# Optimization experiments

Measured on AMD Instinct MI355X. Metric: run time of the kernel, lower is better.

The kernel has to match this reference:

```python
import jax, jax.numpy as jnp
import numpy as np

N_NODES = 20000
N_EDGES = 320000
HID = 128          # hidden_dim
IN_DIM = 192       # edge_rep feature dim
NODE_IN = 64       # node_feature dim


def _w(key, shape, fan_in):
    return jax.random.normal(key, shape, dtype=jnp.float32) * (1.0 / np.sqrt(fan_in))


def setup_inputs() -> dict:
    key = jax.random.key(0)
    ks = jax.random.split(key, 16)
    edge_index = jax.random.randint(ks[0], (2, N_EDGES), 0, N_NODES)
    edge_rep = jax.random.normal(ks[1], (N_EDGES, IN_DIM), dtype=jnp.float32)
    x = jax.random.normal(ks[2], (N_NODES, HID), dtype=jnp.float32)
    prototype = jax.random.normal(ks[3], (N_NODES, HID), dtype=jnp.float32)
    node_feature = jax.random.normal(ks[4], (N_NODES, NODE_IN), dtype=jnp.float32)
    # incidence: each graph edge belongs to the hyperedges of its two endpoint nodes
    inc_edge = jnp.concatenate([jnp.arange(N_EDGES), jnp.arange(N_EDGES)])      # indexes graph edges (conv 'nodes')
    inc_hyper = jnp.concatenate([edge_index[0], edge_index[1]])                 # indexes nodes (hyperedges)
    hyper_edge = jnp.stack([inc_edge, inc_hyper])                               # [2, 2E]
    return {
        "edge_index": edge_index,
        "edge_rep": edge_rep,
        "x": x,
        "hyper_edge": hyper_edge,
        "prototype": prototype,
        "node_feature": node_feature,
        "lin1_W": _w(ks[5], (2 * HID, HID), 2 * HID),
        "lin1_b": jnp.zeros((HID,), jnp.float32),
        "lin2_W": _w(ks[6], (HID, 1), HID),
        "lin2_b": jnp.zeros((1,), jnp.float32),
        "hc1_W": _w(ks[7], (2 * HID, 2 * HID), 2 * HID),
        "hc1_b": jnp.zeros((2 * HID,), jnp.float32),
        "hc2_W": _w(ks[8], (2 * HID, HID), 2 * HID),
        "hc2_b": jnp.zeros((HID,), jnp.float32),
    }


def hyperconv(xh, inc_n, inc_e, w, W, b, n_nodes, n_hyper):
    # X' = D^{-1} H B H^T (X W) + b, with D_i = sum of incidence weights at node i,
    # B_e = 1/|e| (hyperedge degree normalization).
    xh = xh @ W                                                       # [n_nodes, out]
    D = jax.ops.segment_sum(w[:, 0], inc_n, num_segments=n_nodes)
    Dinv = jnp.where(D > 0, 1.0 / D, 0.0)
    B = jax.ops.segment_sum(jnp.ones_like(w[:, 0]), inc_e, num_segments=n_hyper)
    Binv = jnp.where(B > 0, 1.0 / B, 0.0)
    e = jax.ops.segment_sum(Binv[inc_e][:, None] * xh[inc_n], inc_e, num_segments=n_hyper)
    out = Dinv[:, None] * jax.ops.segment_sum(e[inc_n * 0 + inc_e] if False else e[inc_e], inc_n, num_segments=n_nodes)
    return out + b


def reference(edge_index, edge_rep, x, hyper_edge, prototype, node_feature,
              lin1_W, lin1_b, lin2_W, lin2_b, hc1_W, hc1_b, hc2_W, hc2_b):
    E = edge_rep.shape[0]
    N = x.shape[0]
    # gather-concat edge features
    f_u = node_feature[edge_index[0]]
    f_v = node_feature[edge_index[1]]
    er = jnp.concatenate([edge_rep, (f_u + f_v) * 0.5], axis=1)       # [E, 2*HID]
    # per-node scalar weight MLP (dropout = identity in eval mode)
    h = jax.nn.relu(jnp.concatenate([x, prototype], axis=-1) @ lin1_W + lin1_b)
    node_weight = jax.nn.sigmoid(h @ lin2_W + lin2_b)                 # [N, 1]
    hyper_w = node_weight[hyper_edge[1]]                              # [2E, 1] per-incidence weight
    inc_n, inc_e = hyper_edge[0], hyper_edge[1]
    er = jax.nn.sigmoid(hyperconv(er, inc_n, inc_e, hyper_w, hc1_W, hc1_b, E, N))
    er = jax.nn.sigmoid(hyperconv(er, inc_n, inc_e, hyper_w, hc2_W, hc2_b, E, N))
    return er
```

## Files before the change

### kernel.cpp

```cpp
#include <hip/hip_runtime.h>
#include <math.h>

#define NN 20000
#define NE 320000
#define HID 128
#define IN_DIM 192
#define NODE_IN 64

__device__ __forceinline__ float sigmoidf(float x) {
    return __builtin_amdgcn_rcpf(1.0f + __expf(-x));
}

template<bool CONCAT_A, bool RELU, bool BIAS>
__launch_bounds__(256)
__global__ void gemm_f32(const float* __restrict__ A0, const float* __restrict__ A1,
                         const float* __restrict__ B, const float* __restrict__ bias,
                         float* __restrict__ C, int M, int N, int K)
{
    __shared__ float As[16][68];
    __shared__ float Bs[16][68];
    const int tid = threadIdx.x;
    const int tx = tid & 15;
    const int ty = tid >> 4;
    const int m0 = blockIdx.x * 64;
    const int n0 = blockIdx.y * 64;
    float acc[4][4] = {};

    for (int k0 = 0; k0 < K; k0 += 16) {
        #pragma unroll
        for (int i = 0; i < 4; ++i) {
            int g = tid + i * 256;
            int r = g >> 4;
            int c = g & 15;
            int mr = m0 + r;
            int k  = k0 + c;
            float v = 0.f;
            if (mr < M) {
                if (CONCAT_A) v = (k < 128) ? A0[mr * 128 + k] : A1[mr * 128 + (k - 128)];
                else          v = A0[mr * K + k];
            }
            As[c][r] = v;
        }
        #pragma unroll
        for (int i = 0; i < 4; ++i) {
            int g = tid + i * 256;
            int kr = g >> 6;
            int c  = g & 63;
            Bs[kr][c] = B[(k0 + kr) * N + (n0 + c)];
        }
        __syncthreads();
        #pragma unroll
        for (int kk = 0; kk < 16; ++kk) {
            float4 a = *(const float4*)&As[kk][ty * 4];
            float4 b = *(const float4*)&Bs[kk][tx * 4];
            float av[4] = {a.x, a.y, a.z, a.w};
            float bv[4] = {b.x, b.y, b.z, b.w};
            #pragma unroll
            for (int i = 0; i < 4; ++i)
                #pragma unroll
                for (int j = 0; j < 4; ++j)
                    acc[i][j] = fmaf(av[i], bv[j], acc[i][j]);
        }
        __syncthreads();
    }
    #pragma unroll
    for (int i = 0; i < 4; ++i) {
        int row = m0 + ty * 4 + i;
        if (row < M) {
            #pragma unroll
            for (int j = 0; j < 4; ++j) {
                int col = n0 + tx * 4 + j;
                float v = acc[i][j];
                if (BIAS) v += bias[col];
                if (RELU) v = fmaxf(v, 0.f);
                C[row * N + col] = v;
            }
        }
    }
}

__global__ void nw_kernel(const float* __restrict__ h, const float* __restrict__ W2,
                          const float* __restrict__ b2, float* __restrict__ nw)
{
    int n = blockIdx.x * 4 + (threadIdx.x >> 6);
    int l = threadIdx.x & 63;
    if (n >= NN) return;
    float p = h[n * 128 + l] * W2[l] + h[n * 128 + 64 + l] * W2[64 + l];
    #pragma unroll
    for (int off = 32; off > 0; off >>= 1)
        p += __shfl_down(p, off, 64);
    if (l == 0) nw[n] = sigmoidf(p + b2[0]);
}

__global__ void deg_kernel(const int* __restrict__ ei, int* __restrict__ deg)
{
    int s = blockIdx.x * blockDim.x + threadIdx.x;
    if (s >= 2 * NE) return;
    atomicAdd(&deg[ei[s]], 1);
}

__global__ void dinv_kernel(const int* __restrict__ ei, const float* __restrict__ nw,
                            float* __restrict__ Dinv)
{
    int j = blockIdx.x * blockDim.x + threadIdx.x;
    if (j >= NE) return;
    float d = nw[ei[j]] + nw[ei[NE + j]];
    Dinv[j] = __builtin_amdgcn_rcpf(d);
}

__global__ void scan_kernel(const int* __restrict__ deg, int* __restrict__ off,
                            float* __restrict__ Binv)
{
    __shared__ int part[1024];
    int t = threadIdx.x;
    const int C = (NN + 1023) / 1024;
    int base = t * C;
    int s = 0;
    for (int i = 0; i < C; ++i) {
        int idx = base + i;
        if (idx < NN) s += deg[idx];
    }
    part[t] = s;
    __syncthreads();
    for (int o = 1; o < 1024; o <<= 1) {
        int v = (t >= o) ? part[t - o] : 0;
        __syncthreads();
        part[t] += v;
        __syncthreads();
    }
    int excl = (t == 0) ? 0 : part[t - 1];
    for (int i = 0; i < C; ++i) {
        int idx = base + i;
        if (idx < NN) {
            off[idx] = excl;
            int d = deg[idx];
            excl += d;
            Binv[idx] = (d > 0) ? 1.0f / (float)d : 0.0f;
        }
    }
    if (t == 0) off[NN] = part[1023];
}

__global__ void fill_kernel(const int* __restrict__ ei, const int* __restrict__ off,
                            int* __restrict__ cur, int* __restrict__ csr_j,
                            int* __restrict__ csr_o)
{
    int s = blockIdx.x * blockDim.x + threadIdx.x;
    if (s >= 2 * NE) return;
    int n = ei[s];
    int j = (s < NE) ? s : s - NE;
    int o = ei[(s < NE) ? s + NE : s - NE];
    int p = atomicAdd(&cur[n], 1);
    int w = off[n] + p;
    csr_j[w] = j;
    csr_o[w] = o;
}

__launch_bounds__(256)
__global__ void agg0_kernel(const int* __restrict__ csr_j, const int* __restrict__ csr_o,
                            const int* __restrict__ off, const float* __restrict__ Binv,
                            const float* __restrict__ er, const float* __restrict__ nf,
                            float* __restrict__ agg0)
{
    __shared__ int sh_j[256];
    __shared__ int sh_o[256];
    int n = blockIdx.x;
    int c = threadIdx.x;
    int s0 = off[n], s1 = off[n + 1];
    float a0 = 0.f, a1 = 0.f, a2 = 0.f, a3 = 0.f;
    for (int base = s0; base < s1; base += 256) {
        int cnt = min(256, s1 - base);
        if (c < cnt) {
            sh_j[c] = csr_j[base + c];
            sh_o[c] = csr_o[base + c];
        }
        __syncthreads();
        int t = 0;
        if (c < 192) {
            for (; t + 8 <= cnt; t += 8) {
                float v0 = er[sh_j[t + 0] * 192 + c];
                float v1 = er[sh_j[t + 1] * 192 + c];
                float v2 = er[sh_j[t + 2] * 192 + c];
                float v3 = er[sh_j[t + 3] * 192 + c];
                float v4 = er[sh_j[t + 4] * 192 + c];
                float v5 = er[sh_j[t + 5] * 192 + c];
                float v6 = er[sh_j[t + 6] * 192 + c];
                float v7 = er[sh_j[t + 7] * 192 + c];
                a0 += v0 + v4; a1 += v1 + v5; a2 += v2 + v6; a3 += v3 + v7;
            }
            for (; t < cnt; ++t) a0 += er[sh_j[t] * 192 + c];
        } else {
            int cc = c - 192;
            for (; t + 8 <= cnt; t += 8) {
                float v0 = nf[sh_o[t + 0] * 64 + cc];
                float v1 = nf[sh_o[t + 1] * 64 + cc];
                float v2 = nf[sh_o[t + 2] * 64 + cc];
                float v3 = nf[sh_o[t + 3] * 64 + cc];
                float v4 = nf[sh_o[t + 4] * 64 + cc];
                float v5 = nf[sh_o[t + 5] * 64 + cc];
                float v6 = nf[sh_o[t + 6] * 64 + cc];
                float v7 = nf[sh_o[t + 7] * 64 + cc];
                a0 += v0 + v4; a1 += v1 + v5; a2 += v2 + v6; a3 += v3 + v7;
            }
            for (; t < cnt; ++t) a0 += nf[sh_o[t] * 64 + cc];
        }
        __syncthreads();
    }
    float tot = (a0 + a1) + (a2 + a3);
    if (c >= 192) {
        float deg = (float)(s1 - s0);
        tot = 0.5f * (tot + deg * nf[n * 64 + (c - 192)]);
    }
    agg0[n * 256 + c] = tot * Binv[n];
}

__launch_bounds__(256)
__global__ void agg1_kernel(const int* __restrict__ csr_j, const int* __restrict__ csr_o,
                            const int* __restrict__ off, const float* __restrict__ Binv,
                            const float* __restrict__ Dinv, const float* __restrict__ e1,
                            const float* __restrict__ b1, float* __restrict__ agg1)
{
    __shared__ int sh_o[256];
    __shared__ float sh_d[256];
    int n = blockIdx.x;
    int c = threadIdx.x;
    int s0 = off[n], s1 = off[n + 1];
    float myv = e1[n * 256 + c];
    float bc = b1[c];
    float a0 = 0.f, a1 = 0.f, a2 = 0.f, a3 = 0.f;
    for (int base = s0; base < s1; base += 256) {
        int cnt = min(256, s1 - base);
        if (c < cnt) {
            int jj = csr_j[base + c];
            sh_o[c] = csr_o[base + c];
            sh_d[c] = Dinv[jj];
        }
        __syncthreads();
        int t = 0;
        for (; t + 8 <= cnt; t += 8) {
            float v0 = e1[sh_o[t + 0] * 256 + c];
            float v1 = e1[sh_o[t + 1] * 256 + c];
            float v2 = e1[sh_o[t + 2] * 256 + c];
            float v3 = e1[sh_o[t + 3] * 256 + c];
            float v4 = e1[sh_o[t + 4] * 256 + c];
            float v5 = e1[sh_o[t + 5] * 256 + c];
            float v6 = e1[sh_o[t + 6] * 256 + c];
            float v7 = e1[sh_o[t + 7] * 256 + c];
            a0 += sigmoidf(fmaf(sh_d[t + 0], myv + v0, bc));
            a1 += sigmoidf(fmaf(sh_d[t + 1], myv + v1, bc));
            a2 += sigmoidf(fmaf(sh_d[t + 2], myv + v2, bc));
            a3 += sigmoidf(fmaf(sh_d[t + 3], myv + v3, bc));
            a0 += sigmoidf(fmaf(sh_d[t + 4], myv + v4, bc));
            a1 += sigmoidf(fmaf(sh_d[t + 5], myv + v5, bc));
            a2 += sigmoidf(fmaf(sh_d[t + 6], myv + v6, bc));
            a3 += sigmoidf(fmaf(sh_d[t + 7], myv + v7, bc));
        }
        for (; t < cnt; ++t) {
            float v = e1[sh_o[t] * 256 + c];
            a0 += sigmoidf(fmaf(sh_d[t], myv + v, bc));
        }
        __syncthreads();
    }
    agg1[n * 256 + c] = ((a0 + a1) + (a2 + a3)) * Binv[n];
}

__global__ void out_kernel(const float* __restrict__ e2, const float* __restrict__ Dinv,
                           const int* __restrict__ ei, const float* __restrict__ b2,
                           float* __restrict__ out)
{
    int j = blockIdx.x * 2 + (threadIdx.x >> 7);
    int c = threadIdx.x & 127;
    int u = ei[j], v = ei[NE + j];
    float x = Dinv[j] * (e2[u * 128 + c] + e2[v * 128 + c]) + b2[c];
    out[j * 128 + c] = sigmoidf(x);
}

extern "C" void kernel_launch(void* const* d_in, const int* in_sizes, int n_in,
                              void* d_out, int out_size, void* d_ws, size_t ws_size,
                              hipStream_t stream)
{
    const int*   ei       = (const int*)  d_in[0];
    const float* edge_rep = (const float*)d_in[1];
    const float* x        = (const float*)d_in[2];
    const float* proto    = (const float*)d_in[4];
    const float* nf       = (const float*)d_in[5];
    const float* lin1_W   = (const float*)d_in[6];
    const float* lin1_b   = (const float*)d_in[7];
    const float* lin2_W   = (const float*)d_in[8];
    const float* lin2_b   = (const float*)d_in[9];
    const float* hc1_W    = (const float*)d_in[10];
    const float* hc1_b    = (const float*)d_in[11];
    const float* hc2_W    = (const float*)d_in[12];
    const float* hc2_b    = (const float*)d_in[13];
    float* out = (float*)d_out;

    const int S = 2 * NE;

    char* ws = (char*)d_ws;
    float* nw   = (float*)(ws);
    float* Dinv = (float*)(ws + 81920);
    int*   deg  = (int*)  (ws + 1363968);
    int*   off  = (int*)  (ws + 1445888);
    int*   cur  = (int*)  (ws + 1527808);
    float* Binv = (float*)(ws + 1609728);
    float* e2   = (float*)(ws + 1691648);

    char* ob = (char*)d_out;
    float* agg   = (float*)(ob);
    float* e1    = (float*)(ob + 20971520);
    float* h     = (float*)(ob + 41943040);
    int*   csr_j = (int*)  (ob + 52428800);
    int*   csr_o = (int*)  (ob + 54988800);

    hipMemsetAsync(deg, 0, NN * sizeof(int), stream);
    hipMemsetAsync(cur, 0, NN * sizeof(int), stream);

    gemm_f32<true, true, true><<<dim3(313, 2), 256, 0, stream>>>(
        x, proto, lin1_W, lin1_b, h, NN, 128, 256);

    nw_kernel<<<5000, 256, 0, stream>>>(h, lin2_W, lin2_b, nw);

    deg_kernel<<<(S + 255) / 256, 256, 0, stream>>>(ei, deg);

    dinv_kernel<<<(NE + 255) / 256, 256, 0, stream>>>(ei, nw, Dinv);

    scan_kernel<<<1, 1024, 0, stream>>>(deg, off, Binv);

    fill_kernel<<<(S + 255) / 256, 256, 0, stream>>>(ei, off, cur, csr_j, csr_o);

    agg0_kernel<<<NN, 256, 0, stream>>>(csr_j, csr_o, off, Binv, edge_rep, nf, agg);

    gemm_f32<false, false, false><<<dim3(313, 4), 256, 0, stream>>>(
        agg, nullptr, hc1_W, nullptr, e1, NN, 256, 256);

    agg1_kernel<<<NN, 256, 0, stream>>>(csr_j, csr_o, off, Binv, Dinv, e1, hc1_b, agg);

    gemm_f32<false, false, false><<<dim3(313, 2), 256, 0, stream>>>(
        agg, nullptr, hc2_W, nullptr, e2, NN, 128, 256);

    out_kernel<<<NE / 2, 256, 0, stream>>>(e2, Dinv, ei, hc2_b, out);
}
```

Measured before the change: 863.3 us.

## Vectorize gather kernels with float4 and enlarge GEMM per-thread tile

The two CSR aggregation kernels now read float4 row chunks, with several edge slots per block handled in parallel and a shared-memory reduction at the end. The output kernel also uses float4 loads and stores. The GEMM drops to 128 threads with a 4x8 register tile and vectorized stores. The aim is fewer, wider memory transactions in the gather-bound stages and more arithmetic per shared-memory load in the GEMM, at the cost of an extra reduction step and more registers per thread.

```diff
diff --git a/kernel.cpp b/kernel.cpp
--- a/kernel.cpp
+++ b/kernel.cpp
@@ -12,7 +12,7 @@
 }
 
 template<bool CONCAT_A, bool RELU, bool BIAS>
-__launch_bounds__(256)
+__launch_bounds__(128)
 __global__ void gemm_f32(const float* __restrict__ A0, const float* __restrict__ A1,
                          const float* __restrict__ B, const float* __restrict__ bias,
                          float* __restrict__ C, int M, int N, int K)
@@ -20,16 +20,16 @@
     __shared__ float As[16][68];
     __shared__ float Bs[16][68];
     const int tid = threadIdx.x;
-    const int tx = tid & 15;
-    const int ty = tid >> 4;
+    const int tx = tid & 7;
+    const int ty = tid >> 3;
     const int m0 = blockIdx.x * 64;
     const int n0 = blockIdx.y * 64;
-    float acc[4][4] = {};
+    float acc[4][8] = {};
 
     for (int k0 = 0; k0 < K; k0 += 16) {
         #pragma unroll
-        for (int i = 0; i < 4; ++i) {
-            int g = tid + i * 256;
+        for (int i = 0; i < 8; ++i) {
+            int g = tid + i * 128;
             int r = g >> 4;
             int c = g & 15;
             int mr = m0 + r;
@@ -42,8 +42,8 @@
             As[c][r] = v;
         }
         #pragma unroll
-        for (int i = 0; i < 4; ++i) {
-            int g = tid + i * 256;
+        for (int i = 0; i < 8; ++i) {
+            int g = tid + i * 128;
             int kr = g >> 6;
             int c  = g & 63;
             Bs[kr][c] = B[(k0 + kr) * N + (n0 + c)];
@@ -51,14 +51,15 @@
         __syncthreads();
         #pragma unroll
         for (int kk = 0; kk < 16; ++kk) {
-            float4 a = *(const float4*)&As[kk][ty * 4];
-            float4 b = *(const float4*)&Bs[kk][tx * 4];
+            float4 a  = *(const float4*)&As[kk][ty * 4];
+            float4 b0 = *(const float4*)&Bs[kk][tx * 8];
+            float4 b1 = *(const float4*)&Bs[kk][tx * 8 + 4];
             float av[4] = {a.x, a.y, a.z, a.w};
-            float bv[4] = {b.x, b.y, b.z, b.w};
+            float bv[8] = {b0.x, b0.y, b0.z, b0.w, b1.x, b1.y, b1.z, b1.w};
             #pragma unroll
             for (int i = 0; i < 4; ++i)
                 #pragma unroll
-                for (int j = 0; j < 4; ++j)
+                for (int j = 0; j < 8; ++j)
                     acc[i][j] = fmaf(av[i], bv[j], acc[i][j]);
         }
         __syncthreads();
@@ -67,14 +68,24 @@
     for (int i = 0; i < 4; ++i) {
         int row = m0 + ty * 4 + i;
         if (row < M) {
-            #pragma unroll
-            for (int j = 0; j < 4; ++j) {
-                int col = n0 + tx * 4 + j;
-                float v = acc[i][j];
-                if (BIAS) v += bias[col];
-                if (RELU) v = fmaxf(v, 0.f);
-                C[row * N + col] = v;
-            }
+            int col = n0 + tx * 8;
+            float4 v0, v1;
+            v0.x = acc[i][0]; v0.y = acc[i][1]; v0.z = acc[i][2]; v0.w = acc[i][3];
+            v1.x = acc[i][4]; v1.y = acc[i][5]; v1.z = acc[i][6]; v1.w = acc[i][7];
+            if (BIAS) {
+                float4 bb0 = *(const float4*)&bias[col];
+                float4 bb1 = *(const float4*)&bias[col + 4];
+                v0.x += bb0.x; v0.y += bb0.y; v0.z += bb0.z; v0.w += bb0.w;
+                v1.x += bb1.x; v1.y += bb1.y; v1.z += bb1.z; v1.w += bb1.w;
+            }
+            if (RELU) {
+                v0.x = fmaxf(v0.x, 0.f); v0.y = fmaxf(v0.y, 0.f);
+                v0.z = fmaxf(v0.z, 0.f); v0.w = fmaxf(v0.w, 0.f);
+                v1.x = fmaxf(v1.x, 0.f); v1.y = fmaxf(v1.y, 0.f);
+                v1.z = fmaxf(v1.z, 0.f); v1.w = fmaxf(v1.w, 0.f);
+            }
+            *(float4*)&C[row * N + col]     = v0;
+            *(float4*)&C[row * N + col + 4] = v1;
         }
     }
 }
@@ -164,54 +175,81 @@
 {
     __shared__ int sh_j[256];
     __shared__ int sh_o[256];
-    int n = blockIdx.x;
-    int c = threadIdx.x;
-    int s0 = off[n], s1 = off[n + 1];
-    float a0 = 0.f, a1 = 0.f, a2 = 0.f, a3 = 0.f;
+    __shared__ float4 sh_acc[256];
+    const int n = blockIdx.x;
+    const int tid = threadIdx.x;
+    const bool is_er = tid < 192;
+    int grp, slot;
+    if (is_er) { grp = tid % 48;          slot = tid / 48; }
+    else       { grp = (tid - 192) & 15;  slot = (tid - 192) >> 4; }
+    const int s0 = off[n], s1 = off[n + 1];
+    float4 acc = make_float4(0.f, 0.f, 0.f, 0.f);
+
     for (int base = s0; base < s1; base += 256) {
         int cnt = min(256, s1 - base);
-        if (c < cnt) {
-            sh_j[c] = csr_j[base + c];
-            sh_o[c] = csr_o[base + c];
-        }
-        __syncthreads();
-        int t = 0;
-        if (c < 192) {
-            for (; t + 8 <= cnt; t += 8) {
-                float v0 = er[sh_j[t + 0] * 192 + c];
-                float v1 = er[sh_j[t + 1] * 192 + c];
-                float v2 = er[sh_j[t + 2] * 192 + c];
-                float v3 = er[sh_j[t + 3] * 192 + c];
-                float v4 = er[sh_j[t + 4] * 192 + c];
-                float v5 = er[sh_j[t + 5] * 192 + c];
-                float v6 = er[sh_j[t + 6] * 192 + c];
-                float v7 = er[sh_j[t + 7] * 192 + c];
-                a0 += v0 + v4; a1 += v1 + v5; a2 += v2 + v6; a3 += v3 + v7;
-            }
-            for (; t < cnt; ++t) a0 += er[sh_j[t] * 192 + c];
+        if (tid < cnt) {
+            sh_j[tid] = csr_j[base + tid];
+            sh_o[tid] = csr_o[base + tid];
+        }
+        __syncthreads();
+        if (is_er) {
+            int t = slot;
+            for (; t + 4 < cnt; t += 8) {
+                float4 v0 = *(const float4*)&er[(size_t)sh_j[t] * 192 + grp * 4];
+                float4 v1 = *(const float4*)&er[(size_t)sh_j[t + 4] * 192 + grp * 4];
+                acc.x += v0.x + v1.x; acc.y += v0.y + v1.y;
+                acc.z += v0.z + v1.z; acc.w += v0.w + v1.w;
+            }
+            if (t < cnt) {
+                float4 v = *(const float4*)&er[(size_t)sh_j[t] * 192 + grp * 4];
+                acc.x += v.x; acc.y += v.y; acc.z += v.z; acc.w += v.w;
+            }
         } else {
-            int cc = c - 192;
-            for (; t + 8 <= cnt; t += 8) {
-                float v0 = nf[sh_o[t + 0] * 64 + cc];
-                float v1 = nf[sh_o[t + 1] * 64 + cc];
-                float v2 = nf[sh_o[t + 2] * 64 + cc];
-                float v3 = nf[sh_o[t + 3] * 64 + cc];
-                float v4 = nf[sh_o[t + 4] * 64 + cc];
-                float v5 = nf[sh_o[t + 5] * 64 + cc];
-                float v6 = nf[sh_o[t + 6] * 64 + cc];
-                float v7 = nf[sh_o[t + 7] * 64 + cc];
-                a0 += v0 + v4; a1 += v1 + v5; a2 += v2 + v6; a3 += v3 + v7;
-            }
-            for (; t < cnt; ++t) a0 += nf[sh_o[t] * 64 + cc];
-        }
-        __syncthreads();
-    }
-    float tot = (a0 + a1) + (a2 + a3);
-    if (c >= 192) {
-        float deg = (float)(s1 - s0);
-        tot = 0.5f * (tot + deg * nf[n * 64 + (c - 192)]);
-    }
-    agg0[n * 256 + c] = tot * Binv[n];
+            int t = slot;
+            for (; t + 4 < cnt; t += 8) {
+                float4 v0 = *(const float4*)&nf[(size_t)sh_o[t] * 64 + grp * 4];
+                float4 v1 = *(const float4*)&nf[(size_t)sh_o[t + 4] * 64 + grp * 4];
+                acc.x += v0.x + v1.x; acc.y += v0.y + v1.y;
+                acc.z += v0.z + v1.z; acc.w += v0.w + v1.w;
+            }
+            if (t < cnt) {
+                float4 v = *(const float4*)&nf[(size_t)sh_o[t] * 64 + grp * 4];
+                acc.x += v.x; acc.y += v.y; acc.z += v.z; acc.w += v.w;
+            }
+        }
+        __syncthreads();
+    }
+
+    sh_acc[tid] = acc;
+    __syncthreads();
+    if (tid < 64) {
+        float4 tot;
+        if (tid < 48) {
+            float4 p0 = sh_acc[tid], p1 = sh_acc[tid + 48];
+            float4 p2 = sh_acc[tid + 96], p3 = sh_acc[tid + 144];
+            tot.x = (p0.x + p1.x) + (p2.x + p3.x);
+            tot.y = (p0.y + p1.y) + (p2.y + p3.y);
+            tot.z = (p0.z + p1.z) + (p2.z + p3.z);
+            tot.w = (p0.w + p1.w) + (p2.w + p3.w);
+        } else {
+            int b = 192 + (tid - 48);
+            float4 p0 = sh_acc[b], p1 = sh_acc[b + 16];
+            float4 p2 = sh_acc[b + 32], p3 = sh_acc[b + 48];
+            tot.x = (p0.x + p1.x) + (p2.x + p3.x);
+            tot.y = (p0.y + p1.y) + (p2.y + p3.y);
+            tot.z = (p0.z + p1.z) + (p2.z + p3.z);
+            tot.w = (p0.w + p1.w) + (p2.w + p3.w);
+            float degf = (float)(s1 - s0);
+            float4 nfn = *(const float4*)&nf[(size_t)n * 64 + (tid - 48) * 4];
+            tot.x = 0.5f * (tot.x + degf * nfn.x);
+            tot.y = 0.5f * (tot.y + degf * nfn.y);
+            tot.z = 0.5f * (tot.z + degf * nfn.z);
+            tot.w = 0.5f * (tot.w + degf * nfn.w);
+        }
+        float bi = Binv[n];
+        tot.x *= bi; tot.y *= bi; tot.z *= bi; tot.w *= bi;
+        *(float4*)&agg0[(size_t)n * 256 + tid * 4] = tot;
+    }
 }
 
 __launch_bounds__(256)
@@ -222,57 +260,82 @@
 {
     __shared__ int sh_o[256];
     __shared__ float sh_d[256];
-    int n = blockIdx.x;
-    int c = threadIdx.x;
-    int s0 = off[n], s1 = off[n + 1];
-    float myv = e1[n * 256 + c];
-    float bc = b1[c];
-    float a0 = 0.f, a1 = 0.f, a2 = 0.f, a3 = 0.f;
+    __shared__ float4 sh_acc[256];
+    const int n = blockIdx.x;
+    const int tid = threadIdx.x;
+    const int cg = tid & 63;
+    const int slot = tid >> 6;
+    const int s0 = off[n], s1 = off[n + 1];
+    float4 myv = *(const float4*)&e1[(size_t)n * 256 + cg * 4];
+    float4 bc  = *(const float4*)&b1[cg * 4];
+    float4 acc = make_float4(0.f, 0.f, 0.f, 0.f);
+
     for (int base = s0; base < s1; base += 256) {
         int cnt = min(256, s1 - base);
-        if (c < cnt) {
-            int jj = csr_j[base + c];
-            sh_o[c] = csr_o[base + c];
-            sh_d[c] = Dinv[jj];
-        }
-        __syncthreads();
-        int t = 0;
-        for (; t + 8 <= cnt; t += 8) {
-            float v0 = e1[sh_o[t + 0] * 256 + c];
-            float v1 = e1[sh_o[t + 1] * 256 + c];
-            float v2 = e1[sh_o[t + 2] * 256 + c];
-            float v3 = e1[sh_o[t + 3] * 256 + c];
-            float v4 = e1[sh_o[t + 4] * 256 + c];
-            float v5 = e1[sh_o[t + 5] * 256 + c];
-            float v6 = e1[sh_o[t + 6] * 256 + c];
-            float v7 = e1[sh_o[t + 7] * 256 + c];
-            a0 += sigmoidf(fmaf(sh_d[t + 0], myv + v0, bc));
-            a1 += sigmoidf(fmaf(sh_d[t + 1], myv + v1, bc));
-            a2 += sigmoidf(fmaf(sh_d[t + 2], myv + v2, bc));
-            a3 += sigmoidf(fmaf(sh_d[t + 3], myv + v3, bc));
-            a0 += sigmoidf(fmaf(sh_d[t + 4], myv + v4, bc));
-            a1 += sigmoidf(fmaf(sh_d[t + 5], myv + v5, bc));
-            a2 += sigmoidf(fmaf(sh_d[t + 6], myv + v6, bc));
-            a3 += sigmoidf(fmaf(sh_d[t + 7], myv + v7, bc));
-        }
-        for (; t < cnt; ++t) {
-            float v = e1[sh_o[t] * 256 + c];
-            a0 += sigmoidf(fmaf(sh_d[t], myv + v, bc));
-        }
-        __syncthreads();
-    }
-    agg1[n * 256 + c] = ((a0 + a1) + (a2 + a3)) * Binv[n];
+        if (tid < cnt) {
+            int jj = csr_j[base + tid];
+            sh_o[tid] = csr_o[base + tid];
+            sh_d[tid] = Dinv[jj];
+        }
+        __syncthreads();
+        int t = slot;
+        for (; t + 4 < cnt; t += 8) {
+            int o0 = sh_o[t], o1 = sh_o[t + 4];
+            float d0 = sh_d[t], d1 = sh_d[t + 4];
+            float4 v0 = *(const float4*)&e1[(size_t)o0 * 256 + cg * 4];
+            float4 v1 = *(const float4*)&e1[(size_t)o1 * 256 + cg * 4];
+            acc.x += sigmoidf(fmaf(d0, myv.x + v0.x, bc.x));
+            acc.y += sigmoidf(fmaf(d0, myv.y + v0.y, bc.y));
+            acc.z += sigmoidf(fmaf(d0, myv.z + v0.z, bc.z));
+            acc.w += sigmoidf(fmaf(d0, myv.w + v0.w, bc.w));
+            acc.x += sigmoidf(fmaf(d1, myv.x + v1.x, bc.x));
+            acc.y += sigmoidf(fmaf(d1, myv.y + v1.y, bc.y));
+            acc.z += sigmoidf(fmaf(d1, myv.z + v1.z, bc.z));
+            acc.w += sigmoidf(fmaf(d1, myv.w + v1.w, bc.w));
+        }
+        if (t < cnt) {
+            int o0 = sh_o[t];
+            float d0 = sh_d[t];
+            float4 v0 = *(const float4*)&e1[(size_t)o0 * 256 + cg * 4];
+            acc.x += sigmoidf(fmaf(d0, myv.x + v0.x, bc.x));
+            acc.y += sigmoidf(fmaf(d0, myv.y + v0.y, bc.y));
+            acc.z += sigmoidf(fmaf(d0, myv.z + v0.z, bc.z));
+            acc.w += sigmoidf(fmaf(d0, myv.w + v0.w, bc.w));
+        }
+        __syncthreads();
+    }
+
+    sh_acc[tid] = acc;
+    __syncthreads();
+    if (tid < 64) {
+        float4 p1 = sh_acc[tid + 64], p2 = sh_acc[tid + 128], p3 = sh_acc[tid + 192];
+        float bi = Binv[n];
+        float4 outv;
+        outv.x = ((acc.x + p1.x) + (p2.x + p3.x)) * bi;
+        outv.y = ((acc.y + p1.y) + (p2.y + p3.y)) * bi;
+        outv.z = ((acc.z + p1.z) + (p2.z + p3.z)) * bi;
+        outv.w = ((acc.w + p1.w) + (p2.w + p3.w)) * bi;
+        *(float4*)&agg1[(size_t)n * 256 + tid * 4] = outv;
+    }
 }
 
 __global__ void out_kernel(const float* __restrict__ e2, const float* __restrict__ Dinv,
                            const int* __restrict__ ei, const float* __restrict__ b2,
                            float* __restrict__ out)
 {
-    int j = blockIdx.x * 2 + (threadIdx.x >> 7);
-    int c = threadIdx.x & 127;
+    int j = blockIdx.x * 8 + (threadIdx.x >> 5);
+    int cg = threadIdx.x & 31;
     int u = ei[j], v = ei[NE + j];
-    float x = Dinv[j] * (e2[u * 128 + c] + e2[v * 128 + c]) + b2[c];
-    out[j * 128 + c] = sigmoidf(x);
+    float d = Dinv[j];
+    float4 a  = *(const float4*)&e2[(size_t)u * 128 + cg * 4];
+    float4 b  = *(const float4*)&e2[(size_t)v * 128 + cg * 4];
+    float4 bb = *(const float4*)&b2[cg * 4];
+    float4 r;
+    r.x = sigmoidf(fmaf(d, a.x + b.x, bb.x));
+    r.y = sigmoidf(fmaf(d, a.y + b.y, bb.y));
+    r.z = sigmoidf(fmaf(d, a.z + b.z, bb.z));
+    r.w = sigmoidf(fmaf(d, a.w + b.w, bb.w));
+    *(float4*)&out[(size_t)j * 128 + cg * 4] = r;
 }
 
 extern "C" void kernel_launch(void* const* d_in, const int* in_sizes, int n_in,
@@ -315,7 +378,7 @@
     hipMemsetAsync(deg, 0, NN * sizeof(int), stream);
     hipMemsetAsync(cur, 0, NN * sizeof(int), stream);
 
-    gemm_f32<true, true, true><<<dim3(313, 2), 256, 0, stream>>>(
+    gemm_f32<true, true, true><<<dim3(313, 2), 128, 0, stream>>>(
         x, proto, lin1_W, lin1_b, h, NN, 128, 256);
 
     nw_kernel<<<5000, 256, 0, stream>>>(h, lin2_W, lin2_b, nw);
@@ -330,13 +393,13 @@
 
     agg0_kernel<<<NN, 256, 0, stream>>>(csr_j, csr_o, off, Binv, edge_rep, nf, agg);
 
-    gemm_f32<false, false, false><<<dim3(313, 4), 256, 0, stream>>>(
+    gemm_f32<false, false, false><<<dim3(313, 4), 128, 0, stream>>>(
         agg, nullptr, hc1_W, nullptr, e1, NN, 256, 256);
 
     agg1_kernel<<<NN, 256, 0, stream>>>(csr_j, csr_o, off, Binv, Dinv, e1, hc1_b, agg);
 
-    gemm_f32<false, false, false><<<dim3(313, 2), 256, 0, stream>>>(
+    gemm_f32<false, false, false><<<dim3(313, 2), 128, 0, stream>>>(
         agg, nullptr, hc2_W, nullptr, e2, NN, 128, 256);
 
-    out_kernel<<<NE / 2, 256, 0, stream>>>(e2, Dinv, ei, hc2_b, out);
-}
+    out_kernel<<<NE / 8, 256, 0, stream>>>(e2, Dinv, ei, hc2_b, out);
+}
```

Result: slower. 881.1 us (+2.1%).
